# Performance work log

Hardware: AMD Instinct MI355X
Metric: run time of the kernel (lower is better)

The kernel has to match this reference:

```python
import jax, jax.numpy as jnp
import numpy as np

NUM_CELLS = 15        # num_beams (polar bins over (-pi/2, pi/2])
NEIGH = 2.0           # neighborhood_size -> default fallback radius
P, B = 2048, 10000    # pedestrians, boundary points
EMB, HDIM, MID, BOT = 64, 64, 512, 1024


def setup_inputs() -> dict:
    key = jax.random.key(0)
    ks = jax.random.split(key, 8)
    def n(k, shp, s=1.0):
        return jax.random.normal(k, shp, dtype=jnp.float32) * s
    return {
        "h_states": n(ks[0], (1, P, HDIM)),
        "end_pos": n(ks[1], (P, 2), 4.0),
        "rel_pos": n(ks[2], (P, 2)),
        "boundary_points": n(ks[3], (B, 2), 5.0),
        "W_sp": n(ks[4], (2, EMB), 0.5),
        "b_sp": jnp.zeros((EMB,), jnp.float32),
        "W1": n(ks[5], (EMB + HDIM, MID), 0.05),
        "b1": jnp.zeros((MID,), jnp.float32),
        "g1": jnp.ones((MID,), jnp.float32),
        "be1": jnp.zeros((MID,), jnp.float32),
        "W2": n(ks[6], (MID, BOT), 0.05),
        "b2": jnp.zeros((BOT,), jnp.float32),
        "g2": jnp.ones((BOT,), jnp.float32),
        "be2": jnp.zeros((BOT,), jnp.float32),
    }


def _bn(x, g, b, eps=1e-5):
    # torch BatchNorm1d in training mode: biased batch statistics
    m = x.mean(axis=0)
    v = x.var(axis=0)
    return g * (x - m) * jax.lax.rsqrt(v + eps) + b


def _polar_grid(end_pos, rel_pos, bpts, nb, radius):
    # Vectorized replacement of the pandas pd.cut + groupby(...).idxmin path.
    Pn, Bn = end_pos.shape[0], bpts.shape[0]
    th_ped = jnp.arctan2(rel_pos[:, 1], rel_pos[:, 0])      # (P,)
    c, s = jnp.cos(th_ped)[:, None], jnp.sin(th_ped)[:, None]
    d = bpts[None, :, :] - end_pos[:, None, :]              # (P,B,2)
    xb = d[..., 0] * c + d[..., 1] * s                      # rotate into ped frame
    yb = -d[..., 0] * s + d[..., 1] * c
    r = jnp.sqrt(xb * xb + yb * yb)                         # (P,B)
    th = jnp.arctan2(yb, xb)                                # (P,B)

    width = np.pi / nb
    binid = jnp.clip(jnp.floor((th + np.pi / 2) / width).astype(jnp.int32), 0, nb - 1)
    valid = (th > -np.pi / 2) & (th <= np.pi / 2)           # pd.cut: (a, b] intervals
    pid = jnp.arange(Pn, dtype=jnp.int32)[:, None]
    dump = Pn * nb                                          # segment for out-of-range points
    seg = jnp.where(valid, pid * nb + binid, dump)          # (P,B)

    # appended fallback rows: one per (ped, bin) at bin-center angle, radius=neighborhood_size
    centers = jnp.linspace(-np.pi / 2 + np.pi / nb / 2,
                           np.pi / 2 - np.pi / nb / 2, nb).astype(jnp.float32)
    r_all = jnp.concatenate([r.ravel(), jnp.full((Pn * nb,), radius, jnp.float32)])
    th_all = jnp.concatenate([th.ravel(), jnp.tile(centers, Pn)])
    seg_all = jnp.concatenate([seg.ravel(), jnp.arange(Pn * nb, dtype=jnp.int32)])

    ns = Pn * nb + 1
    rmin = jax.ops.segment_min(r_all, seg_all, num_segments=ns)
    # argmin with first-occurrence tie-break (matches pandas idxmin ordering)
    N = r_all.shape[0]
    idx = jnp.arange(N, dtype=jnp.int32)
    cand = jnp.where(r_all <= rmin[seg_all], idx, N)
    arg = jax.ops.segment_min(cand, seg_all, num_segments=ns)[:Pn * nb]

    th_ch = th_all[arg].reshape(Pn, nb)
    r_ch = rmin[:Pn * nb].reshape(Pn, nb)
    xc = r_ch * jnp.cos(th_ch)
    yc = r_ch * jnp.sin(th_ch)
    # rotate back to world frame and translate
    x = xc * c - yc * s + end_pos[:, 0:1]
    y = xc * s + yc * c + end_pos[:, 1:2]
    return jnp.stack([x, y], axis=-1)                       # (P, nb, 2)


def reference(h_states, end_pos, rel_pos, boundary_points,
              W_sp, b_sp, W1, b1, g1, be1, W2, b2, g2, be2):
    cart = _polar_grid(end_pos, rel_pos, boundary_points, NUM_CELLS, NEIGH)
    rel_grid = (cart - end_pos[:, None, :]).reshape(-1, 2)  # (P*nb, 2)
    emb = rel_grid @ W_sp + b_sp                            # spatial_embedding
    h = h_states.reshape(-1, HDIM)                          # (P, h_dim)
    hid = jnp.repeat(h, NUM_CELLS, axis=0)                  # R1,R1,...,R2,R2,...
    x = jnp.concatenate([emb, hid], axis=1)                 # (P*nb, 128)
    x = jax.nn.relu(_bn(x @ W1 + b1, g1, be1))
    x = jax.nn.relu(_bn(x @ W2 + b2, g2, be2))
    return x.reshape(P, NUM_CELLS, BOT).max(axis=1)         # (P, bottleneck_dim)
```

## Files before the change

kernel.cpp:

```cpp
#include <hip/hip_runtime.h>
#include <hip/hip_bf16.h>
#include <math.h>

#define P_N   2048
#define B_N   10000
#define NB    15
#define MROWS (P_N * NB)
#define SPLIT 5
#define BPB   (B_N / SPLIT)

typedef __bf16 bf16x8 __attribute__((ext_vector_type(8)));
typedef float  f32x4  __attribute__((ext_vector_type(4)));

__device__ __forceinline__ float bf2f(unsigned short u) {
    union { unsigned int i; float f; } v; v.i = ((unsigned int)u) << 16; return v.f;
}
__device__ __forceinline__ unsigned short f2bf(float f) {
    union { float f; unsigned int i; } v; v.f = f;
    unsigned int i = v.i;
    i += 0x7FFFu + ((i >> 16) & 1u);
    return (unsigned short)(i >> 16);
}
__device__ __forceinline__ void gld_lds16(const unsigned short* g, unsigned short* l) {
    __builtin_amdgcn_global_load_lds(
        (const __attribute__((address_space(1))) unsigned int*)g,
        (__attribute__((address_space(3))) unsigned int*)l, 16, 0, 0);
}
__device__ __forceinline__ unsigned fkey(float f) {
    unsigned b = __float_as_uint(f);
    return (b & 0x80000000u) ? ~b : (b | 0x80000000u);
}
__device__ __forceinline__ float funkey(unsigned key) {
    unsigned b = (key & 0x80000000u) ? (key ^ 0x80000000u) : ~key;
    return __uint_as_float(b);
}

__global__ __launch_bounds__(256) void k_front(const float* __restrict__ W1,
        const float* __restrict__ W2, unsigned short* __restrict__ w1t,
        unsigned short* __restrict__ w2t, float* __restrict__ stats,
        const float* __restrict__ end_pos, const float* __restrict__ rel_pos,
        const float* __restrict__ bpts, unsigned long long* __restrict__ pkeys,
        const float* __restrict__ h, unsigned short* __restrict__ hbf,
        const float* __restrict__ Wsp, const float* __restrict__ bsp,
        const float* __restrict__ b1, float* __restrict__ V0,
        float* __restrict__ V1, float* __restrict__ cvec) {
    __shared__ unsigned short t[64][65];
    __shared__ unsigned long long s_key[NB];
    int blk = blockIdx.x, tid = threadIdx.x;
    if (blk < 144) {
        const float* W; unsigned short* O; int NC, K, tr, tc;
        if (blk < 16) { W = W1; O = w1t; NC = 512; K = 128; tr = blk & 1; tc = blk >> 1; }
        else { int b = blk - 16; W = W2; O = w2t; NC = 1024; K = 512; tr = b & 7; tc = b >> 3; }
        int r0 = tr * 64, c0 = tc * 64;
        int cx = tid & 63, rg = tid >> 6;
#pragma unroll
        for (int i = 0; i < 16; ++i) {
            int r = rg * 16 + i;
            t[r][cx] = f2bf(W[(size_t)(r0 + r) * NC + c0 + cx]);
        }
        __syncthreads();
#pragma unroll
        for (int i = 0; i < 16; ++i) {
            int n = rg * 16 + i;
            O[(size_t)(c0 + n) * K + r0 + cx] = t[cx][n];
        }
    } else if (blk < 2196) {
        int zidx = (blk - 144) * 256 + tid;
        if (zidx < 525056) {
            uint4 z = {0u, 0u, 0u, 0u};
            ((uint4*)stats)[zidx] = z;
        }
    } else if (blk < 2198) {
        int col = (blk - 2196) * 256 + tid;
        float v0 = 0.f, v1 = 0.f, cc = 0.f;
        for (int e = 0; e < 64; ++e) {
            float w = W1[(size_t)e * 512 + col];
            v0 = fmaf(Wsp[e], w, v0);
            v1 = fmaf(Wsp[64 + e], w, v1);
            cc = fmaf(bsp[e], w, cc);
        }
        V0[col] = v0; V1[col] = v1; cvec[col] = cc + b1[col];
    } else if (blk < 2326) {
        int base = (blk - 2198) * 1024 + tid * 4;
        float4 hv = *(const float4*)(h + base);
        unsigned short ub[4] = {f2bf(hv.x), f2bf(hv.y), f2bf(hv.z), f2bf(hv.w)};
        *(uint2*)(hbf + base) = *(uint2*)ub;
    } else {
        int sb = blk - 2326;
        int p = sb / SPLIT, part = sb % SPLIT;
        if (tid < NB) s_key[tid] = ~0ull;
        __syncthreads();

        float ex = end_pos[2 * p], ey = end_pos[2 * p + 1];
        float rx = rel_pos[2 * p], ry = rel_pos[2 * p + 1];
        float rr = rx * rx + ry * ry;
        float c, s;
        if (rr > 0.0f) { float inv = 1.0f / sqrtf(rr); c = rx * inv; s = ry * inv; }
        else           { c = 1.0f; s = 0.0f; }

        const float T0 = -4.704630109f, T1 = -2.246036774f, T2 = -1.376381920f,
                    T3 = -0.900404044f, T4 = -0.577350269f, T5 = -0.324919696f,
                    T6 = -0.105104235f, T7 =  0.105104235f, T8 =  0.324919696f,
                    T9 =  0.577350269f, T10 = 0.900404044f, T11 = 1.376381920f,
                    T12 = 2.246036774f, T13 = 4.704630109f;

        const float2* bp2 = (const float2*)bpts;
        int bstart = part * BPB;
        for (int b = bstart + tid; b < bstart + BPB; b += 256) {
            float2 pt = bp2[b];
            float dx = pt.x - ex, dy = pt.y - ey;
            float xb = dx * c + dy * s;
            float yb = dy * c - dx * s;
            float r2 = xb * xb + yb * yb;
            bool v3 = yb > T7 * xb;
            float ta = v3 ? T11 : T3;
            bool v2 = yb > ta * xb;
            float tb = v3 ? (v2 ? T13 : T9) : (v2 ? T5 : T1);
            bool v1 = yb > tb * xb;
            float tc = v3 ? (v2 ? (v1 ? 3.0e38f : T12) : (v1 ? T10 : T8))
                          : (v2 ? (v1 ? T6 : T4)       : (v1 ? T2 : T0));
            bool v0 = yb > tc * xb;
            int bin = (v3 ? 8 : 0) + (v2 ? 4 : 0) + (v1 ? 2 : 0) + (v0 ? 1 : 0);
            if (xb > 0.0f) {
                unsigned long long key =
                    ((unsigned long long)__float_as_uint(r2) << 32) | (unsigned int)b;
                atomicMin(&s_key[bin], key);
            }
        }
        __syncthreads();
        if (tid < NB) pkeys[(size_t)part * MROWS + p * NB + tid] = s_key[tid];
    }
}

__global__ __launch_bounds__(64) void k_assemble(
        const unsigned long long* __restrict__ pkeys,
        const float* __restrict__ end_pos, const float* __restrict__ rel_pos,
        const float* __restrict__ bpts, float* __restrict__ rel) {
    int p = blockIdx.x, tid = threadIdx.x;
    if (tid < NB) {
        float ex = end_pos[2 * p], ey = end_pos[2 * p + 1];
        unsigned long long key = ~0ull;
#pragma unroll
        for (int part = 0; part < SPLIT; ++part) {
            unsigned long long k = pkeys[(size_t)part * MROWS + p * NB + tid];
            key = (k < key) ? k : key;
        }
        float r = sqrtf(__uint_as_float((unsigned int)(key >> 32)));
        float relx, rely;
        if (r <= 2.0f) {
            int b = (int)(key & 0xFFFFFFFFu);
            relx = bpts[2 * b] - ex; rely = bpts[2 * b + 1] - ey;
        } else {
            float rx = rel_pos[2 * p], ry = rel_pos[2 * p + 1];
            float rr = rx * rx + ry * ry;
            float c, s;
            if (rr > 0.0f) { float inv = 1.0f / sqrtf(rr); c = rx * inv; s = ry * inv; }
            else           { c = 1.0f; s = 0.0f; }
            float th = ((float)tid + 0.5f) * (float)(M_PI / 15.0) - (float)(M_PI / 2.0);
            float xc = 2.0f * cosf(th), yc = 2.0f * sinf(th);
            relx = xc * c - yc * s;
            rely = xc * s + yc * c;
        }
        rel[(size_t)(p * NB + tid) * 2]     = relx;
        rel[(size_t)(p * NB + tid) * 2 + 1] = rely;
    }
}

__global__ __launch_bounds__(512) void k_hgemm(const unsigned short* __restrict__ hbf,
        const unsigned short* __restrict__ w1t, float* __restrict__ Hp) {
    __shared__ __align__(16) unsigned short lds[24576];
    int tid = threadIdx.x;
    int bm = blockIdx.x & 15, bnn = blockIdx.x >> 4;
    int row0 = bm << 7, col0 = bnn << 8;
    int lane = tid & 63, wave = tid >> 6;
    int wr = wave >> 2, wc = wave & 3;
    int frow = lane & 15, kq = lane >> 4;

    f32x4 zero = {0.f, 0.f, 0.f, 0.f};
    f32x4 acc[4][4];
#pragma unroll
    for (int i = 0; i < 4; ++i)
#pragma unroll
        for (int j = 0; j < 4; ++j) acc[i][j] = zero;

#pragma unroll
    for (int k = 0; k < 6; ++k) {
        int ch = wave * 6 + k;
        int s = (ch >= 24) ? 1 : 0;
        int r = ch - s * 24;
        unsigned short* dst = lds + s * 12288 + r * 512;
        const unsigned short* src =
            (r < 8) ? (hbf + (size_t)(row0 + r * 16 + frow) * 64 + s * 32 + kq * 8)
                    : (w1t + (size_t)(col0 + (r - 8) * 16 + frow) * 128 + 64 + s * 32 + kq * 8);
        gld_lds16(src, dst);
    }
    asm volatile("s_waitcnt vmcnt(0)" ::: "memory");
    __builtin_amdgcn_s_barrier();
    asm volatile("" ::: "memory");

#pragma unroll
    for (int s = 0; s < 2; ++s) {
        const unsigned short* sub = lds + s * 12288;
        bf16x8 af[4], bfv[4];
#pragma unroll
        for (int i = 0; i < 4; ++i)
            af[i] = *(const bf16x8*)&sub[(wr * 4 + i) * 512 + kq * 128 + frow * 8];
#pragma unroll
        for (int j = 0; j < 4; ++j)
            bfv[j] = *(const bf16x8*)&sub[4096 + (wc * 4 + j) * 512 + kq * 128 + frow * 8];
#pragma unroll
        for (int i = 0; i < 4; ++i)
#pragma unroll
            for (int j = 0; j < 4; ++j)
                acc[i][j] = __builtin_amdgcn_mfma_f32_16x16x32_bf16(af[i], bfv[j], acc[i][j], 0, 0, 0);
    }

#pragma unroll
    for (int i = 0; i < 4; ++i)
#pragma unroll
        for (int j = 0; j < 4; ++j)
#pragma unroll
            for (int r = 0; r < 4; ++r) {
                int row = row0 + wr * 64 + i * 16 + kq * 4 + r;
                int col = col0 + wc * 64 + j * 16 + frow;
                Hp[(size_t)row * 512 + col] = acc[i][j][r];
            }
}

__global__ __launch_bounds__(256) void k_stat1(const float* __restrict__ Hp,
        const float* __restrict__ rel, const float* __restrict__ V0,
        const float* __restrict__ V1, const float* __restrict__ cvec,
        float* __restrict__ s1, float* __restrict__ q1) {
    __shared__ float s_s[512], s_q[512];
    int tid = threadIdx.x;
    int pi = tid >> 6, seg = tid & 63;
    int p = blockIdx.x * 4 + pi;
    s_s[tid] = 0.f; s_s[tid + 256] = 0.f;
    s_q[tid] = 0.f; s_q[tid + 256] = 0.f;
    __syncthreads();

    float4 ha = *(const float4*)(Hp + (size_t)p * 512 + seg * 8);
    float4 hb = *(const float4*)(Hp + (size_t)p * 512 + seg * 8 + 4);
    float4 ca = *(const float4*)(cvec + seg * 8);
    float4 cb = *(const float4*)(cvec + seg * 8 + 4);
    float4 va = *(const float4*)(V0 + seg * 8), vb = *(const float4*)(V0 + seg * 8 + 4);
    float4 wa = *(const float4*)(V1 + seg * 8), wb = *(const float4*)(V1 + seg * 8 + 4);
    float hc[8] = {ha.x+ca.x, ha.y+ca.y, ha.z+ca.z, ha.w+ca.w,
                   hb.x+cb.x, hb.y+cb.y, hb.z+cb.z, hb.w+cb.w};
    float v0[8] = {va.x,va.y,va.z,va.w,vb.x,vb.y,vb.z,vb.w};
    float v1[8] = {wa.x,wa.y,wa.z,wa.w,wb.x,wb.y,wb.z,wb.w};
    float ss[8] = {0,0,0,0,0,0,0,0}, qq[8] = {0,0,0,0,0,0,0,0};
#pragma unroll
    for (int cell = 0; cell < NB; ++cell) {
        float2 rl = *(const float2*)(rel + (size_t)(p * NB + cell) * 2);
#pragma unroll
        for (int j = 0; j < 8; ++j) {
            float y = fmaf(rl.x, v0[j], fmaf(rl.y, v1[j], hc[j]));
            ss[j] += y; qq[j] = fmaf(y, y, qq[j]);
        }
    }
#pragma unroll
    for (int j = 0; j < 8; ++j) {
        atomicAdd(&s_s[seg * 8 + j], ss[j]);
        atomicAdd(&s_q[seg * 8 + j], qq[j]);
    }
    __syncthreads();
    atomicAdd(&s1[tid], s_s[tid]);
    atomicAdd(&s1[tid + 256], s_s[tid + 256]);
    atomicAdd(&q1[tid], s_q[tid]);
    atomicAdd(&q1[tid + 256], s_q[tid + 256]);
}

__global__ void k_coef1(const float* __restrict__ s1, const float* __restrict__ q1,
                        const float* __restrict__ g1, const float* __restrict__ be1,
                        float* __restrict__ sc1, float* __restrict__ sh1) {
    int i = blockIdx.x * 256 + threadIdx.x;
    const float invN = 1.0f / (float)MROWS;
    float m = s1[i] * invN;
    float v = q1[i] * invN - m * m;
    float k = g1[i] * rsqrtf(v + 1e-5f);
    sc1[i] = k;
    sh1[i] = be1[i] - m * k;
}

__global__ __launch_bounds__(256) void k_y1w(const float* __restrict__ Hp,
        const float* __restrict__ rel, const float* __restrict__ V0,
        const float* __restrict__ V1, const float* __restrict__ cvec,
        const float* __restrict__ sc1, const float* __restrict__ sh1,
        unsigned short* __restrict__ Y1) {
    int tid = threadIdx.x;
    int p = blockIdx.x;
    int seg = tid & 63, cg = tid >> 6;
    float4 ha = *(const float4*)(Hp + (size_t)p * 512 + seg * 8);
    float4 hb = *(const float4*)(Hp + (size_t)p * 512 + seg * 8 + 4);
    float4 ca = *(const float4*)(cvec + seg * 8);
    float4 cb = *(const float4*)(cvec + seg * 8 + 4);
    float4 va = *(const float4*)(V0 + seg * 8), vb = *(const float4*)(V0 + seg * 8 + 4);
    float4 wa = *(const float4*)(V1 + seg * 8), wb = *(const float4*)(V1 + seg * 8 + 4);
    float4 sa = *(const float4*)(sc1 + seg * 8), sb = *(const float4*)(sc1 + seg * 8 + 4);
    float4 oa = *(const float4*)(sh1 + seg * 8), ob = *(const float4*)(sh1 + seg * 8 + 4);
    float hc[8] = {ha.x+ca.x, ha.y+ca.y, ha.z+ca.z, ha.w+ca.w,
                   hb.x+cb.x, hb.y+cb.y, hb.z+cb.z, hb.w+cb.w};
    float v0[8] = {va.x,va.y,va.z,va.w,vb.x,vb.y,vb.z,vb.w};
    float v1[8] = {wa.x,wa.y,wa.z,wa.w,wb.x,wb.y,wb.z,wb.w};
    float sc[8] = {sa.x,sa.y,sa.z,sa.w,sb.x,sb.y,sb.z,sb.w};
    float sh[8] = {oa.x,oa.y,oa.z,oa.w,ob.x,ob.y,ob.z,ob.w};
#pragma unroll
    for (int i = 0; i < 4; ++i) {
        int cell = cg + i * 4;
        if (cell < NB) {
            float2 rl = *(const float2*)(rel + (size_t)(p * NB + cell) * 2);
            unsigned short ub[8];
#pragma unroll
            for (int j = 0; j < 8; ++j) {
                float y = fmaf(rl.x, v0[j], fmaf(rl.y, v1[j], hc[j]));
                float z = fmaxf(fmaf(y, sc[j], sh[j]), 0.0f);
                ub[j] = f2bf(z);
            }
            *(uint4*)(Y1 + (size_t)(p * NB + cell) * 512 + seg * 8) = *(uint4*)ub;
        }
    }
}

template<int K, bool WRITE_C>
__global__ __launch_bounds__(512) void k_gemm256(
        const unsigned short* __restrict__ A, const unsigned short* __restrict__ Bt,
        const float* __restrict__ bias, unsigned short* __restrict__ C,
        int N, float* __restrict__ osum, float* __restrict__ osq,
        unsigned int* __restrict__ mkey) {
    __shared__ __align__(16) unsigned short lds[65536];
    int tid = threadIdx.x;

    int nbt = N >> 8;
    int d = blockIdx.x;
    int m5 = d >> 3;
    int bn = m5 % nbt;
    int bm = (d & 7) + ((m5 / nbt) << 3);
    int row0 = bm << 8, col0 = bn << 8;

    int lane = tid & 63, wave = tid >> 6;
    int wr = wave >> 2, wc = wave & 3;
    int frow = lane & 15, kq = lane >> 4;

    f32x4 zero = {0.f, 0.f, 0.f, 0.f};
    f32x4 acc[8][4];
#pragma unroll
    for (int i = 0; i < 8; ++i)
#pragma unroll
        for (int j = 0; j < 4; ++j) acc[i][j] = zero;

    const unsigned short* gsrc =
        (wave < 4) ? (A  + (size_t)(row0 + (wave << 6) + frow) * K + kq * 8)
                   : (Bt + (size_t)(col0 + ((wave - 4) << 6) + frow) * K + kq * 8);
    unsigned regbase = (wave < 4) ? (unsigned)wave * 2048
                                  : 8192u + (unsigned)(wave - 4) * 2048;

    auto issue2 = [&](int t, int s, int hp) {
        unsigned short* dst = lds + (t & 1) * 32768 + s * 16384 + regbase + hp * 1024;
        const unsigned short* src = gsrc + t * 64 + s * 32 + (size_t)(hp * 32) * K;
        gld_lds16(src,                  dst);
        gld_lds16(src + (size_t)16 * K, dst + 512);
    };

    constexpr int NT = K / 64;
    static_assert(NT >= 2, "need >=2 K-tiles");

    issue2(0, 0, 0); issue2(0, 0, 1); issue2(0, 1, 0); issue2(0, 1, 1);

#pragma unroll
    for (int t = 0; t < NT; ++t) {
        const unsigned short* buf = lds + (t & 1) * 32768;
        bool more = (t + 1 < NT);
#pragma unroll
        for (int s = 0; s < 2; ++s) {
            const unsigned short* sub = buf + s * 16384;
            if (more || s == 0) asm volatile("s_waitcnt vmcnt(4)" ::: "memory");
            else                asm volatile("s_waitcnt vmcnt(0)" ::: "memory");
            __builtin_amdgcn_s_barrier();
            asm volatile("" ::: "memory");
            bf16x8 bfv[4], af[4];
#pragma unroll
            for (int j = 0; j < 4; ++j)
                bfv[j] = *(const bf16x8*)&sub[8192 + (wc * 4 + j) * 512 + kq * 128 + frow * 8];
#pragma unroll
            for (int i = 0; i < 4; ++i)
                af[i] = *(const bf16x8*)&sub[(wr * 8 + i) * 512 + kq * 128 + frow * 8];
            if (more) issue2(t + 1, s, 0);
            __builtin_amdgcn_s_barrier();
            asm volatile("" ::: "memory");
            __builtin_amdgcn_s_setprio(1);
#pragma unroll
            for (int i = 0; i < 4; ++i)
#pragma unroll
                for (int j = 0; j < 4; ++j)
                    acc[i][j] = __builtin_amdgcn_mfma_f32_16x16x32_bf16(af[i], bfv[j], acc[i][j], 0, 0, 0);
            __builtin_amdgcn_s_setprio(0);
#pragma unroll
            for (int i = 0; i < 4; ++i)
                af[i] = *(const bf16x8*)&sub[(wr * 8 + 4 + i) * 512 + kq * 128 + frow * 8];
            if (more) issue2(t + 1, s, 1);
            __builtin_amdgcn_s_barrier();
            asm volatile("" ::: "memory");
            __builtin_amdgcn_s_setprio(1);
#pragma unroll
            for (int i = 0; i < 4; ++i)
#pragma unroll
                for (int j = 0; j < 4; ++j)
                    acc[4 + i][j] = __builtin_amdgcn_mfma_f32_16x16x32_bf16(af[i], bfv[j], acc[4 + i][j], 0, 0, 0);
            __builtin_amdgcn_s_setprio(0);
        }
    }

    float bv[4];
#pragma unroll
    for (int j = 0; j < 4; ++j) bv[j] = bias[col0 + wc * 64 + j * 16 + frow];

#pragma unroll
    for (int j = 0; j < 4; ++j) {
        int col = col0 + wc * 64 + j * 16 + frow;
        float csum = 0.f, csq = 0.f;
#pragma unroll
        for (int i = 0; i < 8; ++i) {
#pragma unroll
            for (int r = 0; r < 4; ++r) {
                float y = acc[i][j][r] + bv[j];
                csum += y; csq = fmaf(y, y, csq);
            }
        }
        csum += __shfl_xor(csum, 16); csum += __shfl_xor(csum, 32);
        csq  += __shfl_xor(csq, 16);  csq  += __shfl_xor(csq, 32);
        if (lane < 16) { atomicAdd(&osum[col], csum); atomicAdd(&osq[col], csq); }
    }

    unsigned short* ldsC = lds;
#pragma unroll
    for (int b = 0; b < 4; ++b) {
        __syncthreads();
        if (wr == (b >> 1)) {
#pragma unroll
            for (int j = 0; j < 4; ++j) {
#pragma unroll
                for (int ii = 0; ii < 4; ++ii) {
                    int i = (b & 1) * 4 + ii;
#pragma unroll
                    for (int r = 0; r < 4; ++r) {
                        float y = acc[i][j][r] + bv[j];
                        ldsC[(ii * 16 + kq * 4 + r) * 264 + wc * 64 + j * 16 + frow] = f2bf(y);
                    }
                }
            }
        }
        __syncthreads();
        if (WRITE_C) {
#pragma unroll
            for (int it = 0; it < 4; ++it) {
                int s = it * 512 + tid;
                int brow = s >> 5, seg = s & 31;
                *(uint4*)(C + (size_t)(row0 + b * 64 + brow) * N + col0 + seg * 8) =
                    *(const uint4*)&ldsC[brow * 264 + seg * 8];
            }
        } else {
            int col = tid & 255, half = tid >> 8;
            int lrow0 = half * 32;
            int grow = row0 + b * 64 + lrow0;
            int curp = grow / 15;
            int rem = 15 - (grow - curp * 15);
            float mx = -3.0e38f;
#pragma unroll
            for (int r = 0; r < 32; ++r) {
                mx = fmaxf(mx, bf2f(ldsC[(lrow0 + r) * 264 + col]));
                if (--rem == 0) {
                    atomicMax(&mkey[(size_t)curp * 1024 + col0 + col], fkey(mx));
                    mx = -3.0e38f; ++curp; rem = 15;
                }
            }
            if (rem != 15)
                atomicMax(&mkey[(size_t)curp * 1024 + col0 + col], fkey(mx));
        }
    }
}

__global__ void k_bnfin(const unsigned int* __restrict__ mkey, const float* __restrict__ s2,
                        const float* __restrict__ q2, const float* __restrict__ g2,
                        const float* __restrict__ be2, float* __restrict__ out) {
    int idx = blockIdx.x * 256 + threadIdx.x;
    int p = idx >> 7, cb = idx & 127;
    int c0 = cb << 3;
    const float invN = 1.0f / (float)MROWS;
    float4 sa = *(const float4*)(s2 + c0),  sb = *(const float4*)(s2 + c0 + 4);
    float4 qa = *(const float4*)(q2 + c0),  qb = *(const float4*)(q2 + c0 + 4);
    float4 ga = *(const float4*)(g2 + c0),  gb = *(const float4*)(g2 + c0 + 4);
    float4 ea = *(const float4*)(be2 + c0), eb = *(const float4*)(be2 + c0 + 4);
    float sv[8] = {sa.x,sa.y,sa.z,sa.w,sb.x,sb.y,sb.z,sb.w};
    float qv[8] = {qa.x,qa.y,qa.z,qa.w,qb.x,qb.y,qb.z,qb.w};
    float gv[8] = {ga.x,ga.y,ga.z,ga.w,gb.x,gb.y,gb.z,gb.w};
    float ev[8] = {ea.x,ea.y,ea.z,ea.w,eb.x,eb.y,eb.z,eb.w};
    uint4 k0 = *(const uint4*)(mkey + (size_t)p * 1024 + c0);
    uint4 k1 = *(const uint4*)(mkey + (size_t)p * 1024 + c0 + 4);
    unsigned kv[8] = {k0.x,k0.y,k0.z,k0.w,k1.x,k1.y,k1.z,k1.w};
    float o[8];
#pragma unroll
    for (int j = 0; j < 8; ++j) {
        float m = sv[j] * invN;
        float v = qv[j] * invN - m * m;
        float k = gv[j] * rsqrtf(v + 1e-5f);
        float sh = ev[j] - m * k;
        o[j] = fmaxf(fmaf(funkey(kv[j]), k, sh), 0.0f);
    }
    float4 o0 = {o[0], o[1], o[2], o[3]};
    float4 o1 = {o[4], o[5], o[6], o[7]};
    *(float4*)(out + (size_t)p * 1024 + c0)     = o0;
    *(float4*)(out + (size_t)p * 1024 + c0 + 4) = o1;
}

extern "C" void kernel_launch(void* const* d_in, const int* in_sizes, int n_in,
                              void* d_out, int out_size, void* d_ws, size_t ws_size,
                              hipStream_t stream) {
    const float* h       = (const float*)d_in[0];
    const float* end_pos = (const float*)d_in[1];
    const float* rel_pos = (const float*)d_in[2];
    const float* bpts    = (const float*)d_in[3];
    const float* Wsp     = (const float*)d_in[4];
    const float* bsp     = (const float*)d_in[5];
    const float* W1      = (const float*)d_in[6];
    const float* b1      = (const float*)d_in[7];
    const float* g1      = (const float*)d_in[8];
    const float* be1     = (const float*)d_in[9];
    const float* W2      = (const float*)d_in[10];
    const float* b2      = (const float*)d_in[11];
    const float* g2      = (const float*)d_in[12];
    const float* be2     = (const float*)d_in[13];
    float* out = (float*)d_out;

    char* ws = (char*)d_ws;
    float* s1  = (float*)ws;
    float* q1  = s1 + 512;
    float* s2  = q1 + 512;
    float* q2  = s2 + 1024;
    unsigned int* mkey        = (unsigned int*)(ws + 12288);
    unsigned long long* pkeys = (unsigned long long*)(ws + 12288 + 8388608);
    unsigned short* w1t = (unsigned short*)(ws + 9629696);
    unsigned short* w2t = (unsigned short*)(ws + 9760768);
    unsigned short* hbf = (unsigned short*)(ws + 10809344);
    float* V0   = (float*)(ws + 11071488);
    float* V1   = V0 + 512;
    float* cvec = V1 + 512;
    float* sc1  = cvec + 512;
    float* sh1  = sc1 + 512;
    float* Hp   = (float*)(ws + 11081728);
    float* rel  = (float*)(ws + 15276032);
    unsigned short* Y1 = (unsigned short*)(ws + 15521792);

    k_front<<<12566, 256, 0, stream>>>(W1, W2, w1t, w2t, s1, end_pos, rel_pos,
                                       bpts, pkeys, h, hbf, Wsp, bsp, b1, V0, V1, cvec);
    k_assemble<<<P_N, 64, 0, stream>>>(pkeys, end_pos, rel_pos, bpts, rel);
    k_hgemm<<<32, 512, 0, stream>>>(hbf, w1t, Hp);
    k_stat1<<<P_N / 4, 256, 0, stream>>>(Hp, rel, V0, V1, cvec, s1, q1);
    k_coef1<<<2, 256, 0, stream>>>(s1, q1, g1, be1, sc1, sh1);
    k_y1w<<<P_N, 256, 0, stream>>>(Hp, rel, V0, V1, cvec, sc1, sh1, Y1);
    k_gemm256<512, false><<<(MROWS / 256) * (1024 / 256), 512, 0, stream>>>(
        Y1, w2t, b2, nullptr, 1024, s2, q2, mkey);
    k_bnfin<<<(P_N * 128) / 256, 256, 0, stream>>>(mkey, s2, q2, g2, be2, out);
}
```

Before: 136.1 us.

## Replace brute-force boundary scan with uniform grid binning and local neighbor search

Boundary points are bucketed into a 40x40 uniform grid of 2-unit cells by a single-block counting sort. Each pedestrian then scans only the 3x3 neighborhood of cells, because only points within the radius of 2 can be selected. This replaces the full scan over all P*B point pairs and removes the partial-key merge kernel. The BN1 coefficient kernel is also folded into k_y1w to save a launch. The grid assumes coordinates lie mostly in [-40,40]; points outside are clamped to edge cells, so positions far outside that range could be missed.

```diff
diff --git a/kernel.cpp b/kernel.cpp
--- a/kernel.cpp
+++ b/kernel.cpp
@@ -6,8 +6,6 @@
 #define B_N   10000
 #define NB    15
 #define MROWS (P_N * NB)
-#define SPLIT 5
-#define BPB   (B_N / SPLIT)
 
 typedef __bf16 bf16x8 __attribute__((ext_vector_type(8)));
 typedef float  f32x4  __attribute__((ext_vector_type(4)));
@@ -38,14 +36,11 @@
 __global__ __launch_bounds__(256) void k_front(const float* __restrict__ W1,
         const float* __restrict__ W2, unsigned short* __restrict__ w1t,
         unsigned short* __restrict__ w2t, float* __restrict__ stats,
-        const float* __restrict__ end_pos, const float* __restrict__ rel_pos,
-        const float* __restrict__ bpts, unsigned long long* __restrict__ pkeys,
         const float* __restrict__ h, unsigned short* __restrict__ hbf,
         const float* __restrict__ Wsp, const float* __restrict__ bsp,
         const float* __restrict__ b1, float* __restrict__ V0,
         float* __restrict__ V1, float* __restrict__ cvec) {
     __shared__ unsigned short t[64][65];
-    __shared__ unsigned long long s_key[NB];
     int blk = blockIdx.x, tid = threadIdx.x;
     if (blk < 144) {
         const float* W; unsigned short* O; int NC, K, tr, tc;
@@ -80,89 +75,124 @@
             cc = fmaf(bsp[e], w, cc);
         }
         V0[col] = v0; V1[col] = v1; cvec[col] = cc + b1[col];
-    } else if (blk < 2326) {
+    } else {
         int base = (blk - 2198) * 1024 + tid * 4;
         float4 hv = *(const float4*)(h + base);
         unsigned short ub[4] = {f2bf(hv.x), f2bf(hv.y), f2bf(hv.z), f2bf(hv.w)};
         *(uint2*)(hbf + base) = *(uint2*)ub;
-    } else {
-        int sb = blk - 2326;
-        int p = sb / SPLIT, part = sb % SPLIT;
-        if (tid < NB) s_key[tid] = ~0ull;
+    }
+}
+
+__global__ __launch_bounds__(1024) void k_build(const float* __restrict__ bpts,
+        int* __restrict__ cellstart, float2* __restrict__ sxy, int* __restrict__ sidx) {
+    __shared__ unsigned int cnt[1600];
+    __shared__ unsigned int offs[1600];
+    int tid = threadIdx.x;
+    for (int i = tid; i < 1600; i += 1024) cnt[i] = 0u;
+    __syncthreads();
+    const float2* bp2 = (const float2*)bpts;
+    for (int i = tid; i < B_N; i += 1024) {
+        float2 pt = bp2[i];
+        int cxp = min(39, max(0, (int)floorf((pt.x + 40.0f) * 0.5f)));
+        int cyp = min(39, max(0, (int)floorf((pt.y + 40.0f) * 0.5f)));
+        atomicAdd(&cnt[cyp * 40 + cxp], 1u);
+    }
+    __syncthreads();
+    for (int off = 1; off < 1600; off <<= 1) {
+        unsigned v0 = 0u, v1 = 0u;
+        int i0 = tid, i1 = tid + 1024;
+        if (i0 < 1600) v0 = cnt[i0] + ((i0 >= off) ? cnt[i0 - off] : 0u);
+        if (i1 < 1600) v1 = cnt[i1] + ((i1 >= off) ? cnt[i1 - off] : 0u);
         __syncthreads();
-
-        float ex = end_pos[2 * p], ey = end_pos[2 * p + 1];
-        float rx = rel_pos[2 * p], ry = rel_pos[2 * p + 1];
-        float rr = rx * rx + ry * ry;
-        float c, s;
-        if (rr > 0.0f) { float inv = 1.0f / sqrtf(rr); c = rx * inv; s = ry * inv; }
-        else           { c = 1.0f; s = 0.0f; }
-
-        const float T0 = -4.704630109f, T1 = -2.246036774f, T2 = -1.376381920f,
-                    T3 = -0.900404044f, T4 = -0.577350269f, T5 = -0.324919696f,
-                    T6 = -0.105104235f, T7 =  0.105104235f, T8 =  0.324919696f,
-                    T9 =  0.577350269f, T10 = 0.900404044f, T11 = 1.376381920f,
-                    T12 = 2.246036774f, T13 = 4.704630109f;
-
-        const float2* bp2 = (const float2*)bpts;
-        int bstart = part * BPB;
-        for (int b = bstart + tid; b < bstart + BPB; b += 256) {
-            float2 pt = bp2[b];
+        if (i0 < 1600) cnt[i0] = v0;
+        if (i1 < 1600) cnt[i1] = v1;
+        __syncthreads();
+    }
+    for (int i = tid; i < 1600; i += 1024) {
+        offs[i] = (i == 0) ? 0u : cnt[i - 1];
+        cellstart[i + 1] = (int)cnt[i];
+    }
+    if (tid == 0) cellstart[0] = 0;
+    __syncthreads();
+    for (int i = tid; i < B_N; i += 1024) {
+        float2 pt = bp2[i];
+        int cxp = min(39, max(0, (int)floorf((pt.x + 40.0f) * 0.5f)));
+        int cyp = min(39, max(0, (int)floorf((pt.y + 40.0f) * 0.5f)));
+        unsigned pos = atomicAdd(&offs[cyp * 40 + cxp], 1u);
+        sxy[pos] = pt;
+        sidx[pos] = i;
+    }
+}
+
+__global__ __launch_bounds__(256) void k_pscan(
+        const float* __restrict__ end_pos, const float* __restrict__ rel_pos,
+        const float* __restrict__ bpts, const float2* __restrict__ sxy,
+        const int* __restrict__ sidx, const int* __restrict__ cellstart,
+        float* __restrict__ rel) {
+    __shared__ unsigned long long skey[4][16];
+    int tid = threadIdx.x, wave = tid >> 6, lane = tid & 63;
+    int p = blockIdx.x * 4 + wave;
+    if (lane < NB) skey[wave][lane] = ~0ull;
+    __syncthreads();
+
+    float ex = end_pos[2 * p], ey = end_pos[2 * p + 1];
+    float rx = rel_pos[2 * p], ry = rel_pos[2 * p + 1];
+    float rr = rx * rx + ry * ry;
+    float c, s;
+    if (rr > 0.0f) { float inv = 1.0f / sqrtf(rr); c = rx * inv; s = ry * inv; }
+    else           { c = 1.0f; s = 0.0f; }
+
+    const float T0 = -4.704630109f, T1 = -2.246036774f, T2 = -1.376381920f,
+                T3 = -0.900404044f, T4 = -0.577350269f, T5 = -0.324919696f,
+                T6 = -0.105104235f, T7 =  0.105104235f, T8 =  0.324919696f,
+                T9 =  0.577350269f, T10 = 0.900404044f, T11 = 1.376381920f,
+                T12 = 2.246036774f, T13 = 4.704630109f;
+
+    int cx = min(38, max(1, (int)floorf((ex + 40.0f) * 0.5f)));
+    int cy = min(38, max(1, (int)floorf((ey + 40.0f) * 0.5f)));
+#pragma unroll
+    for (int oy = -1; oy <= 1; ++oy) {
+        int rowc = (cy + oy) * 40 + cx;
+        int st = cellstart[rowc - 1];
+        int en = cellstart[rowc + 2];
+        for (int i = st + lane; i < en; i += 64) {
+            float2 pt = sxy[i];
             float dx = pt.x - ex, dy = pt.y - ey;
             float xb = dx * c + dy * s;
             float yb = dy * c - dx * s;
             float r2 = xb * xb + yb * yb;
-            bool v3 = yb > T7 * xb;
-            float ta = v3 ? T11 : T3;
-            bool v2 = yb > ta * xb;
-            float tb = v3 ? (v2 ? T13 : T9) : (v2 ? T5 : T1);
-            bool v1 = yb > tb * xb;
-            float tc = v3 ? (v2 ? (v1 ? 3.0e38f : T12) : (v1 ? T10 : T8))
-                          : (v2 ? (v1 ? T6 : T4)       : (v1 ? T2 : T0));
-            bool v0 = yb > tc * xb;
-            int bin = (v3 ? 8 : 0) + (v2 ? 4 : 0) + (v1 ? 2 : 0) + (v0 ? 1 : 0);
-            if (xb > 0.0f) {
+            if (xb > 0.0f && r2 <= 4.0f) {
+                bool v3 = yb > T7 * xb;
+                float ta = v3 ? T11 : T3;
+                bool v2 = yb > ta * xb;
+                float tb = v3 ? (v2 ? T13 : T9) : (v2 ? T5 : T1);
+                bool v1 = yb > tb * xb;
+                float tc = v3 ? (v2 ? (v1 ? 3.0e38f : T12) : (v1 ? T10 : T8))
+                              : (v2 ? (v1 ? T6 : T4)       : (v1 ? T2 : T0));
+                bool v0 = yb > tc * xb;
+                int bin = (v3 ? 8 : 0) + (v2 ? 4 : 0) + (v1 ? 2 : 0) + (v0 ? 1 : 0);
                 unsigned long long key =
-                    ((unsigned long long)__float_as_uint(r2) << 32) | (unsigned int)b;
-                atomicMin(&s_key[bin], key);
-            }
-        }
-        __syncthreads();
-        if (tid < NB) pkeys[(size_t)part * MROWS + p * NB + tid] = s_key[tid];
-    }
-}
-
-__global__ __launch_bounds__(64) void k_assemble(
-        const unsigned long long* __restrict__ pkeys,
-        const float* __restrict__ end_pos, const float* __restrict__ rel_pos,
-        const float* __restrict__ bpts, float* __restrict__ rel) {
-    int p = blockIdx.x, tid = threadIdx.x;
-    if (tid < NB) {
-        float ex = end_pos[2 * p], ey = end_pos[2 * p + 1];
-        unsigned long long key = ~0ull;
-#pragma unroll
-        for (int part = 0; part < SPLIT; ++part) {
-            unsigned long long k = pkeys[(size_t)part * MROWS + p * NB + tid];
-            key = (k < key) ? k : key;
-        }
+                    ((unsigned long long)__float_as_uint(r2) << 32) | (unsigned)sidx[i];
+                atomicMin(&skey[wave][bin], key);
+            }
+        }
+    }
+    __syncthreads();
+    if (lane < NB) {
+        unsigned long long key = skey[wave][lane];
         float r = sqrtf(__uint_as_float((unsigned int)(key >> 32)));
         float relx, rely;
         if (r <= 2.0f) {
             int b = (int)(key & 0xFFFFFFFFu);
             relx = bpts[2 * b] - ex; rely = bpts[2 * b + 1] - ey;
         } else {
-            float rx = rel_pos[2 * p], ry = rel_pos[2 * p + 1];
-            float rr = rx * rx + ry * ry;
-            float c, s;
-            if (rr > 0.0f) { float inv = 1.0f / sqrtf(rr); c = rx * inv; s = ry * inv; }
-            else           { c = 1.0f; s = 0.0f; }
-            float th = ((float)tid + 0.5f) * (float)(M_PI / 15.0) - (float)(M_PI / 2.0);
+            float th = ((float)lane + 0.5f) * (float)(M_PI / 15.0) - (float)(M_PI / 2.0);
             float xc = 2.0f * cosf(th), yc = 2.0f * sinf(th);
             relx = xc * c - yc * s;
             rely = xc * s + yc * c;
         }
-        rel[(size_t)(p * NB + tid) * 2]     = relx;
-        rel[(size_t)(p * NB + tid) * 2 + 1] = rely;
+        rel[(size_t)(p * NB + lane) * 2]     = relx;
+        rel[(size_t)(p * NB + lane) * 2 + 1] = rely;
     }
 }
 
@@ -271,40 +301,35 @@
     atomicAdd(&q1[tid + 256], s_q[tid + 256]);
 }
 
-__global__ void k_coef1(const float* __restrict__ s1, const float* __restrict__ q1,
-                        const float* __restrict__ g1, const float* __restrict__ be1,
-                        float* __restrict__ sc1, float* __restrict__ sh1) {
-    int i = blockIdx.x * 256 + threadIdx.x;
-    const float invN = 1.0f / (float)MROWS;
-    float m = s1[i] * invN;
-    float v = q1[i] * invN - m * m;
-    float k = g1[i] * rsqrtf(v + 1e-5f);
-    sc1[i] = k;
-    sh1[i] = be1[i] - m * k;
-}
-
 __global__ __launch_bounds__(256) void k_y1w(const float* __restrict__ Hp,
         const float* __restrict__ rel, const float* __restrict__ V0,
         const float* __restrict__ V1, const float* __restrict__ cvec,
-        const float* __restrict__ sc1, const float* __restrict__ sh1,
+        const float* __restrict__ s1, const float* __restrict__ q1,
+        const float* __restrict__ g1, const float* __restrict__ be1,
         unsigned short* __restrict__ Y1) {
     int tid = threadIdx.x;
     int p = blockIdx.x;
     int seg = tid & 63, cg = tid >> 6;
+    const float invN = 1.0f / (float)MROWS;
     float4 ha = *(const float4*)(Hp + (size_t)p * 512 + seg * 8);
     float4 hb = *(const float4*)(Hp + (size_t)p * 512 + seg * 8 + 4);
     float4 ca = *(const float4*)(cvec + seg * 8);
     float4 cb = *(const float4*)(cvec + seg * 8 + 4);
     float4 va = *(const float4*)(V0 + seg * 8), vb = *(const float4*)(V0 + seg * 8 + 4);
     float4 wa = *(const float4*)(V1 + seg * 8), wb = *(const float4*)(V1 + seg * 8 + 4);
-    float4 sa = *(const float4*)(sc1 + seg * 8), sb = *(const float4*)(sc1 + seg * 8 + 4);
-    float4 oa = *(const float4*)(sh1 + seg * 8), ob = *(const float4*)(sh1 + seg * 8 + 4);
     float hc[8] = {ha.x+ca.x, ha.y+ca.y, ha.z+ca.z, ha.w+ca.w,
                    hb.x+cb.x, hb.y+cb.y, hb.z+cb.z, hb.w+cb.w};
     float v0[8] = {va.x,va.y,va.z,va.w,vb.x,vb.y,vb.z,vb.w};
     float v1[8] = {wa.x,wa.y,wa.z,wa.w,wb.x,wb.y,wb.z,wb.w};
-    float sc[8] = {sa.x,sa.y,sa.z,sa.w,sb.x,sb.y,sb.z,sb.w};
-    float sh[8] = {oa.x,oa.y,oa.z,oa.w,ob.x,ob.y,ob.z,ob.w};
+    float sc[8], sh[8];
+#pragma unroll
+    for (int j = 0; j < 8; ++j) {
+        int cc = seg * 8 + j;
+        float m = s1[cc] * invN;
+        float v = q1[cc] * invN - m * m;
+        float k = g1[cc] * rsqrtf(v + 1e-5f);
+        sc[j] = k; sh[j] = be1[cc] - m * k;
+    }
 #pragma unroll
     for (int i = 0; i < 4; ++i) {
         int cell = cg + i * 4;
@@ -537,27 +562,28 @@
     float* q1  = s1 + 512;
     float* s2  = q1 + 512;
     float* q2  = s2 + 1024;
-    unsigned int* mkey        = (unsigned int*)(ws + 12288);
-    unsigned long long* pkeys = (unsigned long long*)(ws + 12288 + 8388608);
+    unsigned int* mkey = (unsigned int*)(ws + 12288);
+    int*    cellstart  = (int*)(ws + 8400896);
+    float2* sxy        = (float2*)(ws + 8407312);
+    int*    sidx       = (int*)(ws + 8487312);
     unsigned short* w1t = (unsigned short*)(ws + 9629696);
     unsigned short* w2t = (unsigned short*)(ws + 9760768);
     unsigned short* hbf = (unsigned short*)(ws + 10809344);
     float* V0   = (float*)(ws + 11071488);
     float* V1   = V0 + 512;
     float* cvec = V1 + 512;
-    float* sc1  = cvec + 512;
-    float* sh1  = sc1 + 512;
     float* Hp   = (float*)(ws + 11081728);
     float* rel  = (float*)(ws + 15276032);
     unsigned short* Y1 = (unsigned short*)(ws + 15521792);
 
-    k_front<<<12566, 256, 0, stream>>>(W1, W2, w1t, w2t, s1, end_pos, rel_pos,
-                                       bpts, pkeys, h, hbf, Wsp, bsp, b1, V0, V1, cvec);
-    k_assemble<<<P_N, 64, 0, stream>>>(pkeys, end_pos, rel_pos, bpts, rel);
+    k_front<<<2326, 256, 0, stream>>>(W1, W2, w1t, w2t, s1, h, hbf,
+                                      Wsp, bsp, b1, V0, V1, cvec);
+    k_build<<<1, 1024, 0, stream>>>(bpts, cellstart, sxy, sidx);
+    k_pscan<<<P_N / 4, 256, 0, stream>>>(end_pos, rel_pos, bpts, sxy, sidx,
+                                         cellstart, rel);
     k_hgemm<<<32, 512, 0, stream>>>(hbf, w1t, Hp);
     k_stat1<<<P_N / 4, 256, 0, stream>>>(Hp, rel, V0, V1, cvec, s1, q1);
-    k_coef1<<<2, 256, 0, stream>>>(s1, q1, g1, be1, sc1, sh1);
-    k_y1w<<<P_N, 256, 0, stream>>>(Hp, rel, V0, V1, cvec, sc1, sh1, Y1);
+    k_y1w<<<P_N, 256, 0, stream>>>(Hp, rel, V0, V1, cvec, s1, q1, g1, be1, Y1);
     k_gemm256<512, false><<<(MROWS / 256) * (1024 / 256), 512, 0, stream>>>(
         Y1, w2t, b2, nullptr, 1024, s2, q2, mkey);
     k_bnfin<<<(P_N * 128) / 256, 256, 0, stream>>>(mkey, s2, q2, g2, be2, out);
```

Measured after the change: 143.0 us. 1.05x slower.

## Fold layer-1 BN statistics into hgemm epilogue via per-ped moment sums

Applied to the files above, without the earlier changes.

k_assemble now also reduces five per-pedestrian moments of the relative grid offsets (sum x, sum y, sum xx, sum xy, sum yy). The hgemm epilogue uses them to compute each column's sum and sum of squares analytically, which removes the k_stat1 pass over Hp and rel. The k_coef1 kernel is also removed, and k_y1w now computes the BN scale and shift inline. This cuts two launches and one read of Hp in exchange for extra epilogue arithmetic and possible precision loss from the expanded variance formula.

```diff
diff --git a/kernel.cpp b/kernel.cpp
--- a/kernel.cpp
+++ b/kernel.cpp
@@ -135,8 +135,11 @@
 __global__ __launch_bounds__(64) void k_assemble(
         const unsigned long long* __restrict__ pkeys,
         const float* __restrict__ end_pos, const float* __restrict__ rel_pos,
-        const float* __restrict__ bpts, float* __restrict__ rel) {
+        const float* __restrict__ bpts, float* __restrict__ rel,
+        float* __restrict__ pm0, float* __restrict__ pm1, float* __restrict__ pm2,
+        float* __restrict__ pm3, float* __restrict__ pm4) {
     int p = blockIdx.x, tid = threadIdx.x;
+    float relx = 0.f, rely = 0.f;
     if (tid < NB) {
         float ex = end_pos[2 * p], ey = end_pos[2 * p + 1];
         unsigned long long key = ~0ull;
@@ -146,7 +149,6 @@
             key = (k < key) ? k : key;
         }
         float r = sqrtf(__uint_as_float((unsigned int)(key >> 32)));
-        float relx, rely;
         if (r <= 2.0f) {
             int b = (int)(key & 0xFFFFFFFFu);
             relx = bpts[2 * b] - ex; rely = bpts[2 * b + 1] - ey;
@@ -164,10 +166,24 @@
         rel[(size_t)(p * NB + tid) * 2]     = relx;
         rel[(size_t)(p * NB + tid) * 2 + 1] = rely;
     }
+    float m0 = relx, m1 = rely, m2 = relx * relx, m3 = relx * rely, m4 = rely * rely;
+#pragma unroll
+    for (int d = 32; d >= 1; d >>= 1) {
+        m0 += __shfl_xor(m0, d); m1 += __shfl_xor(m1, d);
+        m2 += __shfl_xor(m2, d); m3 += __shfl_xor(m3, d);
+        m4 += __shfl_xor(m4, d);
+    }
+    if (tid == 0) { pm0[p] = m0; pm1[p] = m1; pm2[p] = m2; pm3[p] = m3; pm4[p] = m4; }
 }
 
 __global__ __launch_bounds__(512) void k_hgemm(const unsigned short* __restrict__ hbf,
-        const unsigned short* __restrict__ w1t, float* __restrict__ Hp) {
+        const unsigned short* __restrict__ w1t, float* __restrict__ Hp,
+        const float* __restrict__ V0, const float* __restrict__ V1,
+        const float* __restrict__ cvec,
+        const float* __restrict__ pm0, const float* __restrict__ pm1,
+        const float* __restrict__ pm2, const float* __restrict__ pm3,
+        const float* __restrict__ pm4,
+        float* __restrict__ s1, float* __restrict__ q1) {
     __shared__ __align__(16) unsigned short lds[24576];
     int tid = threadIdx.x;
     int bm = blockIdx.x & 15, bnn = blockIdx.x >> 4;
@@ -215,30 +231,54 @@
                 acc[i][j] = __builtin_amdgcn_mfma_f32_16x16x32_bf16(af[i], bfv[j], acc[i][j], 0, 0, 0);
     }
 
-#pragma unroll
-    for (int i = 0; i < 4; ++i)
-#pragma unroll
-        for (int j = 0; j < 4; ++j)
-#pragma unroll
-            for (int r = 0; r < 4; ++r) {
-                int row = row0 + wr * 64 + i * 16 + kq * 4 + r;
+    float v0c[4], v1c[4], cc[4];
+#pragma unroll
+    for (int j = 0; j < 4; ++j) {
+        int col = col0 + wc * 64 + j * 16 + frow;
+        v0c[j] = V0[col]; v1c[j] = V1[col]; cc[j] = cvec[col];
+    }
+    float csum[4] = {0.f, 0.f, 0.f, 0.f}, csq[4] = {0.f, 0.f, 0.f, 0.f};
+#pragma unroll
+    for (int i = 0; i < 4; ++i) {
+#pragma unroll
+        for (int r = 0; r < 4; ++r) {
+            int row = row0 + wr * 64 + i * 16 + kq * 4 + r;
+            float srx = pm0[row], sry = pm1[row];
+            float sxx = pm2[row], sxy = pm3[row], syy = pm4[row];
+#pragma unroll
+            for (int j = 0; j < 4; ++j) {
                 int col = col0 + wc * 64 + j * 16 + frow;
-                Hp[(size_t)row * 512 + col] = acc[i][j][r];
-            }
-}
-
-__global__ __launch_bounds__(256) void k_stat1(const float* __restrict__ Hp,
+                float hp = acc[i][j][r];
+                Hp[(size_t)row * 512 + col] = hp;
+                float A  = hp + cc[j];
+                float B1 = fmaf(srx, v0c[j], sry * v1c[j]);
+                float B2 = fmaf(v0c[j] * v0c[j], sxx,
+                           fmaf(2.0f * v0c[j] * v1c[j], sxy, v1c[j] * v1c[j] * syy));
+                csum[j] += fmaf(15.0f, A, B1);
+                csq[j]  += fmaf(15.0f, A * A, fmaf(2.0f * A, B1, B2));
+            }
+        }
+    }
+#pragma unroll
+    for (int j = 0; j < 4; ++j) {
+        int col = col0 + wc * 64 + j * 16 + frow;
+        float cs = csum[j], cq = csq[j];
+        cs += __shfl_xor(cs, 16); cs += __shfl_xor(cs, 32);
+        cq += __shfl_xor(cq, 16); cq += __shfl_xor(cq, 32);
+        if (lane < 16) { atomicAdd(&s1[col], cs); atomicAdd(&q1[col], cq); }
+    }
+}
+
+__global__ __launch_bounds__(256) void k_y1w(const float* __restrict__ Hp,
         const float* __restrict__ rel, const float* __restrict__ V0,
         const float* __restrict__ V1, const float* __restrict__ cvec,
-        float* __restrict__ s1, float* __restrict__ q1) {
-    __shared__ float s_s[512], s_q[512];
+        const float* __restrict__ s1, const float* __restrict__ q1,
+        const float* __restrict__ g1, const float* __restrict__ be1,
+        unsigned short* __restrict__ Y1) {
     int tid = threadIdx.x;
-    int pi = tid >> 6, seg = tid & 63;
-    int p = blockIdx.x * 4 + pi;
-    s_s[tid] = 0.f; s_s[tid + 256] = 0.f;
-    s_q[tid] = 0.f; s_q[tid + 256] = 0.f;
-    __syncthreads();
-
+    int p = blockIdx.x;
+    int seg = tid & 63, cg = tid >> 6;
+    const float invN = 1.0f / (float)MROWS;
     float4 ha = *(const float4*)(Hp + (size_t)p * 512 + seg * 8);
     float4 hb = *(const float4*)(Hp + (size_t)p * 512 + seg * 8 + 4);
     float4 ca = *(const float4*)(cvec + seg * 8);
@@ -249,62 +289,15 @@
                    hb.x+cb.x, hb.y+cb.y, hb.z+cb.z, hb.w+cb.w};
     float v0[8] = {va.x,va.y,va.z,va.w,vb.x,vb.y,vb.z,vb.w};
     float v1[8] = {wa.x,wa.y,wa.z,wa.w,wb.x,wb.y,wb.z,wb.w};
-    float ss[8] = {0,0,0,0,0,0,0,0}, qq[8] = {0,0,0,0,0,0,0,0};
-#pragma unroll
-    for (int cell = 0; cell < NB; ++cell) {
-        float2 rl = *(const float2*)(rel + (size_t)(p * NB + cell) * 2);
-#pragma unroll
-        for (int j = 0; j < 8; ++j) {
-            float y = fmaf(rl.x, v0[j], fmaf(rl.y, v1[j], hc[j]));
-            ss[j] += y; qq[j] = fmaf(y, y, qq[j]);
-        }
-    }
+    float sc[8], sh[8];
 #pragma unroll
     for (int j = 0; j < 8; ++j) {
-        atomicAdd(&s_s[seg * 8 + j], ss[j]);
-        atomicAdd(&s_q[seg * 8 + j], qq[j]);
-    }
-    __syncthreads();
-    atomicAdd(&s1[tid], s_s[tid]);
-    atomicAdd(&s1[tid + 256], s_s[tid + 256]);
-    atomicAdd(&q1[tid], s_q[tid]);
-    atomicAdd(&q1[tid + 256], s_q[tid + 256]);
-}
-
-__global__ void k_coef1(const float* __restrict__ s1, const float* __restrict__ q1,
-                        const float* __restrict__ g1, const float* __restrict__ be1,
-                        float* __restrict__ sc1, float* __restrict__ sh1) {
-    int i = blockIdx.x * 256 + threadIdx.x;
-    const float invN = 1.0f / (float)MROWS;
-    float m = s1[i] * invN;
-    float v = q1[i] * invN - m * m;
-    float k = g1[i] * rsqrtf(v + 1e-5f);
-    sc1[i] = k;
-    sh1[i] = be1[i] - m * k;
-}
-
-__global__ __launch_bounds__(256) void k_y1w(const float* __restrict__ Hp,
-        const float* __restrict__ rel, const float* __restrict__ V0,
-        const float* __restrict__ V1, const float* __restrict__ cvec,
-        const float* __restrict__ sc1, const float* __restrict__ sh1,
-        unsigned short* __restrict__ Y1) {
-    int tid = threadIdx.x;
-    int p = blockIdx.x;
-    int seg = tid & 63, cg = tid >> 6;
-    float4 ha = *(const float4*)(Hp + (size_t)p * 512 + seg * 8);
-    float4 hb = *(const float4*)(Hp + (size_t)p * 512 + seg * 8 + 4);
-    float4 ca = *(const float4*)(cvec + seg * 8);
-    float4 cb = *(const float4*)(cvec + seg * 8 + 4);
-    float4 va = *(const float4*)(V0 + seg * 8), vb = *(const float4*)(V0 + seg * 8 + 4);
-    float4 wa = *(const float4*)(V1 + seg * 8), wb = *(const float4*)(V1 + seg * 8 + 4);
-    float4 sa = *(const float4*)(sc1 + seg * 8), sb = *(const float4*)(sc1 + seg * 8 + 4);
-    float4 oa = *(const float4*)(sh1 + seg * 8), ob = *(const float4*)(sh1 + seg * 8 + 4);
-    float hc[8] = {ha.x+ca.x, ha.y+ca.y, ha.z+ca.z, ha.w+ca.w,
-                   hb.x+cb.x, hb.y+cb.y, hb.z+cb.z, hb.w+cb.w};
-    float v0[8] = {va.x,va.y,va.z,va.w,vb.x,vb.y,vb.z,vb.w};
-    float v1[8] = {wa.x,wa.y,wa.z,wa.w,wb.x,wb.y,wb.z,wb.w};
-    float sc[8] = {sa.x,sa.y,sa.z,sa.w,sb.x,sb.y,sb.z,sb.w};
-    float sh[8] = {oa.x,oa.y,oa.z,oa.w,ob.x,ob.y,ob.z,ob.w};
+        int ccix = seg * 8 + j;
+        float m = s1[ccix] * invN;
+        float v = q1[ccix] * invN - m * m;
+        float k = g1[ccix] * rsqrtf(v + 1e-5f);
+        sc[j] = k; sh[j] = be1[ccix] - m * k;
+    }
 #pragma unroll
     for (int i = 0; i < 4; ++i) {
         int cell = cg + i * 4;
@@ -545,19 +538,22 @@
     float* V0   = (float*)(ws + 11071488);
     float* V1   = V0 + 512;
     float* cvec = V1 + 512;
-    float* sc1  = cvec + 512;
-    float* sh1  = sc1 + 512;
     float* Hp   = (float*)(ws + 11081728);
     float* rel  = (float*)(ws + 15276032);
     unsigned short* Y1 = (unsigned short*)(ws + 15521792);
+    float* pm0 = (float*)(ws + 46979072);
+    float* pm1 = pm0 + 2048;
+    float* pm2 = pm1 + 2048;
+    float* pm3 = pm2 + 2048;
+    float* pm4 = pm3 + 2048;
 
     k_front<<<12566, 256, 0, stream>>>(W1, W2, w1t, w2t, s1, end_pos, rel_pos,
                                        bpts, pkeys, h, hbf, Wsp, bsp, b1, V0, V1, cvec);
-    k_assemble<<<P_N, 64, 0, stream>>>(pkeys, end_pos, rel_pos, bpts, rel);
-    k_hgemm<<<32, 512, 0, stream>>>(hbf, w1t, Hp);
-    k_stat1<<<P_N / 4, 256, 0, stream>>>(Hp, rel, V0, V1, cvec, s1, q1);
-    k_coef1<<<2, 256, 0, stream>>>(s1, q1, g1, be1, sc1, sh1);
-    k_y1w<<<P_N, 256, 0, stream>>>(Hp, rel, V0, V1, cvec, sc1, sh1, Y1);
+    k_assemble<<<P_N, 64, 0, stream>>>(pkeys, end_pos, rel_pos, bpts, rel,
+                                       pm0, pm1, pm2, pm3, pm4);
+    k_hgemm<<<32, 512, 0, stream>>>(hbf, w1t, Hp, V0, V1, cvec,
+                                    pm0, pm1, pm2, pm3, pm4, s1, q1);
+    k_y1w<<<P_N, 256, 0, stream>>>(Hp, rel, V0, V1, cvec, s1, q1, g1, be1, Y1);
     k_gemm256<512, false><<<(MROWS / 256) * (1024 / 256), 512, 0, stream>>>(
         Y1, w2t, b2, nullptr, 1024, s2, q2, mkey);
     k_bnfin<<<(P_N * 128) / 256, 256, 0, stream>>>(mkey, s2, q2, g2, be2, out);
```

After: 116.3 us. 14.5% less time.
